# Kernel optimization log

Hardware: AMD Instinct MI355X
Metric: run time of the kernel (lower is better)

## Reference

```python
import jax, jax.numpy as jnp
import numpy as np

N = 40000   # nodes
E = 480000  # edges
F = 128     # input features
H = 128     # hidden
C = 10      # classes
G = 128     # graphs in batch
L = 3       # conv layers
EPS = 1e-5


def _bn(x, g, b):
    # BatchNorm1d, training-mode batch statistics (biased variance, as torch)
    m = x.mean(0)
    v = x.var(0)
    return (x - m) / jnp.sqrt(v + EPS) * g + b


def _gcn_prop(x, row, col, w, n):
    # PyG-style GCN propagation: add self loops (weight 1), sym-normalize, scatter-add.
    loop = jnp.arange(n)
    r = jnp.concatenate([row, loop])
    c = jnp.concatenate([col, loop])
    ww = jnp.concatenate([w, jnp.ones((n,), x.dtype)])
    deg = jax.ops.segment_sum(ww, r, num_segments=n)  # deg >= 1 thanks to self loops
    dinv = jnp.power(deg, -0.5)
    norm = dinv[r] * ww * dinv[c]                      # [E+N]
    return jax.ops.segment_sum(norm[:, None] * x[r], c, num_segments=n)


def setup_inputs() -> dict:
    key = jax.random.key(0)
    ks = jax.random.split(key, 12)
    nrm = lambda k, s: jax.random.normal(k, s, jnp.float32) * 0.02
    return {
        'x': jax.random.normal(ks[0], (N, F), jnp.float32),
        'edge_index': jax.random.randint(ks[1], (2, E), 0, N, jnp.int32),
        'batch': jnp.sort(jax.random.randint(ks[2], (N,), 0, G, jnp.int32)),
        'bn_feat_g': jnp.ones((F,), jnp.float32), 'bn_feat_b': jnp.full((F,), 1e-4, jnp.float32),
        'W_feat': nrm(ks[3], (F, H)),
        'bns_g': jnp.ones((L, H), jnp.float32), 'bns_b': jnp.full((L, H), 1e-4, jnp.float32),
        'conv_W': nrm(ks[4], (L, H, H)), 'conv_b': jnp.zeros((L, H), jnp.float32),
        'W_eatt': nrm(ks[5], (2 * H, 2)), 'b_eatt': jnp.zeros((2,), jnp.float32),
        'W_natt': nrm(ks[6], (H, 2)), 'b_natt': jnp.zeros((2,), jnp.float32),
        'bnc_g': jnp.ones((H,), jnp.float32), 'bnc_b': jnp.full((H,), 1e-4, jnp.float32),
        'bno_g': jnp.ones((H,), jnp.float32), 'bno_b': jnp.full((H,), 1e-4, jnp.float32),
        'Wc': nrm(ks[7], (H, H)), 'bc': jnp.zeros((H,), jnp.float32),
        'Wo': nrm(ks[8], (H, H)), 'bo': jnp.zeros((H,), jnp.float32),
        'ro_bn1_g': jnp.ones((3, H), jnp.float32), 'ro_bn1_b': jnp.full((3, H), 1e-4, jnp.float32),
        'ro_W1': nrm(ks[9], (3, H, H)), 'ro_b1': jnp.zeros((3, H), jnp.float32),
        'ro_bn2_g': jnp.ones((3, H), jnp.float32), 'ro_bn2_b': jnp.full((3, H), 1e-4, jnp.float32),
        'ro_W2': nrm(ks[10], (3, H, C)), 'ro_b2': jnp.zeros((3, C), jnp.float32),
    }


def reference(x, edge_index, batch,
              bn_feat_g, bn_feat_b, W_feat, bns_g, bns_b, conv_W, conv_b,
              W_eatt, b_eatt, W_natt, b_natt, bnc_g, bnc_b, bno_g, bno_b,
              Wc, bc, Wo, bo,
              ro_bn1_g, ro_bn1_b, ro_W1, ro_b1, ro_bn2_g, ro_bn2_b, ro_W2, ro_b2):
    row, col = edge_index[0], edge_index[1]
    # feature BN + gfn conv (linear only, no propagation, no bias) + ReLU
    h = jax.nn.relu(_bn(x, bn_feat_g, bn_feat_b) @ W_feat)
    ones_w = jnp.ones((E,), h.dtype)
    for i in range(L):
        z = _bn(h, bns_g[i], bns_b[i]) @ conv_W[i]
        h = jax.nn.relu(_gcn_prop(z, row, col, ones_w, N) + conv_b[i])
    # edge / node attention
    edge_rep = jnp.concatenate([h[row], h[col]], axis=-1)          # [E, 2H]
    e_att = jax.nn.softmax(edge_rep @ W_eatt + b_eatt, axis=-1)    # [E, 2]
    n_att = jax.nn.softmax(h @ W_natt + b_natt, axis=-1)           # [N, 2]
    xc = n_att[:, 0:1] * h
    xo = n_att[:, 1:2] * h
    xc = jax.nn.relu(_gcn_prop(_bn(xc, bnc_g, bnc_b) @ Wc, row, col, e_att[:, 0], N) + bc)
    xo = jax.nn.relu(_gcn_prop(_bn(xo, bno_g, bno_b) @ Wo, row, col, e_att[:, 1], N) + bo)
    # global add pool -> [G, H]
    xc = jax.ops.segment_sum(xc, batch, num_segments=G)
    xo = jax.ops.segment_sum(xo, batch, num_segments=G)

    def ro(v, i):
        v = _bn(v, ro_bn1_g[i], ro_bn1_b[i]) @ ro_W1[i] + ro_b1[i]
        v = _bn(jax.nn.relu(v), ro_bn2_g[i], ro_bn2_b[i]) @ ro_W2[i] + ro_b2[i]
        return jax.nn.log_softmax(v, axis=-1)

    # with_random=False -> identity permutation; cat_or_add='add' -> xc + xo
    return ro(xc, 0), ro(xo, 1), ro(xc + xo, 2)
```

## Files before the change

### kernel.cpp

```cpp
#include <hip/hip_runtime.h>

#define HD 128

typedef __attribute__((ext_vector_type(8))) short bf16x8v;
typedef __attribute__((ext_vector_type(4))) float f32x4v;

__device__ __forceinline__ unsigned short f2bf(float f) {
  unsigned int u = __float_as_uint(f);
  u += 0x7FFFu + ((u >> 16) & 1u);
  return (unsigned short)(u >> 16);
}
__device__ __forceinline__ float bf2f(unsigned short h) {
  return __uint_as_float(((unsigned int)h) << 16);
}
__device__ __forceinline__ float bflo(unsigned int u) { return __uint_as_float(u << 16); }
__device__ __forceinline__ float bfhi(unsigned int u) { return __uint_as_float(u & 0xFFFF0000u); }
__device__ __forceinline__ unsigned int packbf(float a, float b) {
  return (unsigned int)f2bf(a) | ((unsigned int)f2bf(b) << 16);
}


__global__ void hist_kernel(const int* __restrict__ row, const int* __restrict__ col,
                            int* __restrict__ cnt_in, int* __restrict__ outdeg, int e) {
  int i = blockIdx.x * blockDim.x + threadIdx.x;
  if (i < e) { atomicAdd(&cnt_in[col[i]], 1); atomicAdd(&outdeg[row[i]], 1); }
}

__global__ void scan1(const int* __restrict__ cnt, int n, int* __restrict__ sums) {
  __shared__ int lds[256];
  int b = blockIdx.x, t = threadIdx.x;
  int base = b * 1024 + t * 4;
  int s = 0;
#pragma unroll
  for (int m = 0; m < 4; m++) if (base + m < n) s += cnt[base + m];
  lds[t] = s;
  __syncthreads();
  for (int d = 128; d > 0; d >>= 1) {
    if (t < d) lds[t] += lds[t + d];
    __syncthreads();
  }
  if (t == 0) sums[b] = lds[0];
}

__global__ void scan2(const int* __restrict__ sums, int nc, int* __restrict__ off) {
  int l = threadIdx.x;
  int v = (l < nc) ? sums[l] : 0;
  int x = v;
#pragma unroll
  for (int d = 1; d < 64; d <<= 1) {
    int y = __shfl_up(x, d, 64);
    if (l >= d) x += y;
  }
  if (l < nc) off[l] = x - v;
}

__global__ void scan3(const int* __restrict__ cnt, int n, const int* __restrict__ off,
                      int* __restrict__ ptr, int* __restrict__ cursor) {
  __shared__ int lds[256];
  int b = blockIdx.x, t = threadIdx.x;
  int base = b * 1024 + t * 4;
  int v[4], p[4];
#pragma unroll
  for (int m = 0; m < 4; m++) v[m] = (base + m < n) ? cnt[base + m] : 0;
  p[0] = v[0];
#pragma unroll
  for (int m = 1; m < 4; m++) p[m] = p[m - 1] + v[m];
  int tsum = p[3];
  lds[t] = tsum;
  __syncthreads();
  for (int d = 1; d < 256; d <<= 1) {
    int y = 0;
    if (t >= d) y = lds[t - d];
    __syncthreads();
    lds[t] += y;
    __syncthreads();
  }
  int basev = off[b] + lds[t] - tsum;
  if (b == 0 && t == 0) ptr[0] = 0;
#pragma unroll
  for (int m = 0; m < 4; m++) {
    int i = base + m;
    if (i < n) {
      int incl = basev + p[m];
      ptr[i + 1] = incl;
      cursor[i] = incl - v[m];
    }
  }
}

__global__ void place1(const int* __restrict__ row, const int* __restrict__ col,
                       int* __restrict__ cursor, int* __restrict__ csr_src,
                       int* __restrict__ csr_dst, int* __restrict__ csr_eid, int e) {
  int i = blockIdx.x * blockDim.x + threadIdx.x;
  if (i < e) {
    int c = col[i];
    int pos = atomicAdd(&cursor[c], 1);
    csr_src[pos] = row[i];
    csr_dst[pos] = c;
    csr_eid[pos] = i;
  }
}

__global__ void place2(const int* __restrict__ row, int* __restrict__ cursor2,
                       int* __restrict__ csr2_eid, int e) {
  int i = blockIdx.x * blockDim.x + threadIdx.x;
  if (i < e) {
    int pos = atomicAdd(&cursor2[row[i]], 1);
    csr2_eid[pos] = i;
  }
}

__global__ void dinv1_kernel(const int* __restrict__ outdeg, float* __restrict__ dinv1, int n) {
  int i = blockIdx.x * blockDim.x + threadIdx.x;
  if (i < n) dinv1[i] = rsqrtf((float)(outdeg[i] + 1));
}

__global__ void wn1_flat(const int* __restrict__ csr_src, const int* __restrict__ csr_dst,
                         const float* __restrict__ dinv1, float* __restrict__ wn, int e) {
  int i = blockIdx.x * blockDim.x + threadIdx.x;
  if (i < e) wn[i] = dinv1[csr_src[i]] * dinv1[csr_dst[i]];
}


__global__ void colstats_castx(const float* __restrict__ A, unsigned short* __restrict__ Abf,
                               int n, int rpb, float* __restrict__ sum, float* __restrict__ sumsq) {
  int colj = threadIdx.x & (HD - 1);
  int half = threadIdx.x >> 7;
  int r0 = blockIdx.x * rpb;
  int r1 = min(n, r0 + rpb);
  float s = 0.f, q = 0.f;
  for (int r = r0 + half; r < r1; r += 2) {
    float v = A[(size_t)r * HD + colj];
    Abf[(size_t)r * HD + colj] = f2bf(v);
    s += v; q += v * v;
  }
  atomicAdd(&sum[colj], s);
  atomicAdd(&sumsq[colj], q);
}

__global__ void colstats_bf(const unsigned short* __restrict__ A, int n, int rpb,
                            float* __restrict__ sum, float* __restrict__ sumsq) {
  int colj = threadIdx.x & (HD - 1);
  int half = threadIdx.x >> 7;
  int r0 = blockIdx.x * rpb;
  int r1 = min(n, r0 + rpb);
  float s = 0.f, q = 0.f;
  for (int r = r0 + half; r < r1; r += 2) {
    float v = bf2f(A[(size_t)r * HD + colj]);
    s += v; q += v * v;
  }
  atomicAdd(&sum[colj], s);
  atomicAdd(&sumsq[colj], q);
}

__global__ void colstats_scaled(const unsigned short* __restrict__ A, const float* __restrict__ natt,
                                int n, int rpb, float* __restrict__ o4) {
  int colj = threadIdx.x & (HD - 1);
  int half = threadIdx.x >> 7;
  int r0 = blockIdx.x * rpb;
  int r1 = min(n, r0 + rpb);
  float sc = 0.f, qc = 0.f, so = 0.f, qo = 0.f;
  for (int r = r0 + half; r < r1; r += 2) {
    float v = bf2f(A[(size_t)r * HD + colj]);
    float a0 = natt[r * 2], a1 = natt[r * 2 + 1];
    float vc = a0 * v, vo = a1 * v;
    sc += vc; qc += vc * vc; so += vo; qo += vo * vo;
  }
  atomicAdd(&o4[colj], sc);
  atomicAdd(&o4[HD + colj], qc);
  atomicAdd(&o4[2 * HD + colj], so);
  atomicAdd(&o4[3 * HD + colj], qo);
}


__global__ __launch_bounds__(256) void gemm_mfma(
    const unsigned short* __restrict__ A, const float* __restrict__ W,
    const float* __restrict__ g, const float* __restrict__ b,
    const float* __restrict__ ssum, const float* __restrict__ ssq, float invN,
    const float* __restrict__ rowscale, int rsStride,
    unsigned short* __restrict__ out, int n, int relu) {
  __shared__ unsigned short WT[128][136];
  __shared__ float sA[HD], tA[HD], tb[HD];
  int tid = threadIdx.x;
  int r00 = blockIdx.x * 128;

  if (tid < HD) {
    float m = ssum[tid] * invN;
    float v = ssq[tid] * invN - m * m;
    float s = g[tid] * rsqrtf(v + 1e-5f);
    sA[tid] = s;
    tA[tid] = b[tid] - m * s;
  }
  __syncthreads();
  for (int idx = tid; idx < 4096; idx += 256) {
    int k = idx >> 5;
    int j4 = (idx & 31) * 4;
    float4 w = *(const float4*)(W + (size_t)k * 128 + j4);
    float s = sA[k];
    WT[j4 + 0][k] = f2bf(w.x * s);
    WT[j4 + 1][k] = f2bf(w.y * s);
    WT[j4 + 2][k] = f2bf(w.z * s);
    WT[j4 + 3][k] = f2bf(w.w * s);
  }
  if (tid < HD) {
    float acc = 0.f;
#pragma unroll 8
    for (int k = 0; k < HD; k++) acc += tA[k] * W[(size_t)k * 128 + tid];
    tb[tid] = acc;
  }
  __syncthreads();

  int w = tid >> 6;
  int l = tid & 63;
  int colb = l & 15;
  int kcb = l >> 4;

#pragma unroll
  for (int rt = 0; rt < 2; rt++) {
    int r0 = r00 + rt * 64;
    if (r0 >= n) break;
    int arow = r0 + w * 16 + colb;
    bool rowok = arow < n;

    f32x4v acc[8];
#pragma unroll
    for (int jt = 0; jt < 8; jt++) acc[jt] = (f32x4v){0.f, 0.f, 0.f, 0.f};

    const unsigned short* Ap = A + (size_t)(rowok ? arow : 0) * 128 + kcb * 8;
#pragma unroll
    for (int kit = 0; kit < 4; kit++) {
      bf16x8v a;
      if (rowok) a = *(const bf16x8v*)(Ap + kit * 32);
      else a = (bf16x8v){0, 0, 0, 0, 0, 0, 0, 0};
#pragma unroll
      for (int jt = 0; jt < 8; jt++) {
        bf16x8v bb = *(const bf16x8v*)&WT[jt * 16 + colb][kit * 32 + kcb * 8];
        acc[jt] = __builtin_amdgcn_mfma_f32_16x16x32_bf16(a, bb, acc[jt], 0, 0, 0);
      }
    }

    int rbase = r0 + w * 16 + kcb * 4;
    float rs[4];
#pragma unroll
    for (int i = 0; i < 4; i++)
      rs[i] = rowscale ? ((rbase + i < n) ? rowscale[(size_t)(rbase + i) * rsStride] : 0.f) : 1.f;
#pragma unroll
    for (int jt = 0; jt < 8; jt++) {
      int colj = jt * 16 + colb;
      float tbv = tb[colj];
#pragma unroll
      for (int i = 0; i < 4; i++) {
        int r = rbase + i;
        if (r < n) {
          float v = acc[jt][i] * rs[i] + tbv;
          if (relu) v = fmaxf(v, 0.f);
          out[(size_t)r * 128 + colj] = f2bf(v);
        }
      }
    }
  }
}


__global__ __launch_bounds__(256) void prop1(
    const unsigned short* __restrict__ z, const int* __restrict__ ptr,
    const int* __restrict__ src, const float* __restrict__ wn,
    const float* __restrict__ dinv, const float* __restrict__ bias,
    unsigned short* __restrict__ out, int n, int relu) {
  int node = blockIdx.x * 4 + (threadIdx.x >> 6);
  if (node >= n) return;
  int lane = threadIdx.x & 63;
  const unsigned int* zp = (const unsigned int*)z;
  float dn = dinv[node];
  float ws = dn * dn;
  unsigned int us = zp[(size_t)node * 64 + lane];
  float a0 = ws * bflo(us), a1 = ws * bfhi(us);
  int e = ptr[node], e1 = ptr[node + 1];
  for (; e + 3 < e1; e += 4) {
    int s0 = src[e], s1 = src[e + 1], s2 = src[e + 2], s3 = src[e + 3];
    float w0 = wn[e], w1 = wn[e + 1], w2 = wn[e + 2], w3 = wn[e + 3];
    unsigned int u0 = zp[(size_t)s0 * 64 + lane];
    unsigned int u1 = zp[(size_t)s1 * 64 + lane];
    unsigned int u2 = zp[(size_t)s2 * 64 + lane];
    unsigned int u3 = zp[(size_t)s3 * 64 + lane];
    a0 += w0 * bflo(u0) + w1 * bflo(u1) + w2 * bflo(u2) + w3 * bflo(u3);
    a1 += w0 * bfhi(u0) + w1 * bfhi(u1) + w2 * bfhi(u2) + w3 * bfhi(u3);
  }
  for (; e < e1; e++) {
    unsigned int u = zp[(size_t)src[e] * 64 + lane];
    float we = wn[e];
    a0 += we * bflo(u);
    a1 += we * bfhi(u);
  }
  a0 += bias[lane * 2];
  a1 += bias[lane * 2 + 1];
  if (relu) { a0 = fmaxf(a0, 0.f); a1 = fmaxf(a1, 0.f); }
  ((unsigned int*)out)[(size_t)node * 64 + lane] = packbf(a0, a1);
}

__global__ __launch_bounds__(256) void prop2(
    const unsigned short* __restrict__ z1, const unsigned short* __restrict__ z2,
    const int* __restrict__ ptr, const int* __restrict__ src,
    const float* __restrict__ wnc, const float* __restrict__ wno,
    const float2* __restrict__ ddeg, const float* __restrict__ bc,
    const float* __restrict__ bo, unsigned short* __restrict__ xc,
    unsigned short* __restrict__ xo, int n) {
  int node = blockIdx.x * 4 + (threadIdx.x >> 6);
  if (node >= n) return;
  int lane = threadIdx.x & 63;
  const unsigned int* z1p = (const unsigned int*)z1;
  const unsigned int* z2p = (const unsigned int*)z2;
  float2 dd = ddeg[node];
  float wsc = dd.x * dd.x, wso = dd.y * dd.y;
  unsigned int uc = z1p[(size_t)node * 64 + lane];
  unsigned int uo = z2p[(size_t)node * 64 + lane];
  float c0 = wsc * bflo(uc), c1 = wsc * bfhi(uc);
  float o0 = wso * bflo(uo), o1 = wso * bfhi(uo);
  int e = ptr[node], e1 = ptr[node + 1];
  for (; e + 1 < e1; e += 2) {
    int s0 = src[e], s1 = src[e + 1];
    float wc0 = wnc[e], wc1 = wnc[e + 1];
    float wo0 = wno[e], wo1 = wno[e + 1];
    unsigned int a0 = z1p[(size_t)s0 * 64 + lane];
    unsigned int b0 = z2p[(size_t)s0 * 64 + lane];
    unsigned int a1 = z1p[(size_t)s1 * 64 + lane];
    unsigned int b1 = z2p[(size_t)s1 * 64 + lane];
    c0 += wc0 * bflo(a0) + wc1 * bflo(a1);
    c1 += wc0 * bfhi(a0) + wc1 * bfhi(a1);
    o0 += wo0 * bflo(b0) + wo1 * bflo(b1);
    o1 += wo0 * bfhi(b0) + wo1 * bfhi(b1);
  }
  for (; e < e1; e++) {
    int s = src[e];
    float wc = wnc[e], wo = wno[e];
    unsigned int a = z1p[(size_t)s * 64 + lane];
    unsigned int b = z2p[(size_t)s * 64 + lane];
    c0 += wc * bflo(a); c1 += wc * bfhi(a);
    o0 += wo * bflo(b); o1 += wo * bfhi(b);
  }
  c0 = fmaxf(c0 + bc[lane * 2], 0.f);
  c1 = fmaxf(c1 + bc[lane * 2 + 1], 0.f);
  o0 = fmaxf(o0 + bo[lane * 2], 0.f);
  o1 = fmaxf(o1 + bo[lane * 2 + 1], 0.f);
  ((unsigned int*)xc)[(size_t)node * 64 + lane] = packbf(c0, c1);
  ((unsigned int*)xo)[(size_t)node * 64 + lane] = packbf(o0, o1);
}


__global__ void proj_kernel(const unsigned short* __restrict__ h, const float* __restrict__ We,
                            const float* __restrict__ Wn, const float* __restrict__ bn,
                            float* __restrict__ natt, float* __restrict__ pe, int n) {
  int gtid = blockIdx.x * blockDim.x + threadIdx.x;
  int wave = gtid >> 6;
  int lane = threadIdx.x & 63;
  int nwaves = (gridDim.x * blockDim.x) >> 6;
  for (int node = wave; node < n; node += nwaves) {
    float h0 = bf2f(h[(size_t)node * HD + lane]);
    float h1 = bf2f(h[(size_t)node * HD + 64 + lane]);
    float v[6];
    v[0] = h0 * We[lane * 2 + 0] + h1 * We[(64 + lane) * 2 + 0];
    v[1] = h0 * We[lane * 2 + 1] + h1 * We[(64 + lane) * 2 + 1];
    v[2] = h0 * We[(128 + lane) * 2 + 0] + h1 * We[(192 + lane) * 2 + 0];
    v[3] = h0 * We[(128 + lane) * 2 + 1] + h1 * We[(192 + lane) * 2 + 1];
    v[4] = h0 * Wn[lane * 2 + 0] + h1 * Wn[(64 + lane) * 2 + 0];
    v[5] = h0 * Wn[lane * 2 + 1] + h1 * Wn[(64 + lane) * 2 + 1];
#pragma unroll
    for (int m = 32; m > 0; m >>= 1) {
#pragma unroll
      for (int q = 0; q < 6; q++) v[q] += __shfl_xor(v[q], m, 64);
    }
    if (lane == 0) {
      float q0 = v[4] + bn[0], q1 = v[5] + bn[1];
      float mx = fmaxf(q0, q1);
      float e0 = expf(q0 - mx), e1 = expf(q1 - mx);
      float inv = 1.f / (e0 + e1);
      natt[node * 2 + 0] = e0 * inv;
      natt[node * 2 + 1] = e1 * inv;
      pe[node * 4 + 0] = v[0];
      pe[node * 4 + 1] = v[1];
      pe[node * 4 + 2] = v[2];
      pe[node * 4 + 3] = v[3];
    }
  }
}

__global__ void eatt_flat(const int* __restrict__ row, const int* __restrict__ col,
                          const float* __restrict__ pe, const float* __restrict__ be,
                          float2* __restrict__ eattO, int e) {
  int i = blockIdx.x * blockDim.x + threadIdx.x;
  if (i >= e) return;
  int r = row[i], c = col[i];
  float l0 = pe[r * 4 + 0] + pe[c * 4 + 2] + be[0];
  float l1 = pe[r * 4 + 1] + pe[c * 4 + 3] + be[1];
  float m = fmaxf(l0, l1);
  float e0 = expf(l0 - m), e1 = expf(l1 - m);
  float inv = 1.f / (e0 + e1);
  eattO[i] = make_float2(e0 * inv, e1 * inv);
}

__global__ void deg_kernel(const int* __restrict__ ptrR, const int* __restrict__ csr2_eid,
                           const float2* __restrict__ eattO, float2* __restrict__ ddeg, int n) {
  int gtid = blockIdx.x * blockDim.x + threadIdx.x;
  int node = gtid >> 6;
  int lane = threadIdx.x & 63;
  if (node >= n) return;
  int e0 = ptrR[node], e1 = ptrR[node + 1];
  float sc = 0.f, so = 0.f;
  for (int e = e0 + lane; e < e1; e += 64) {
    float2 at = eattO[csr2_eid[e]];
    sc += at.x; so += at.y;
  }
#pragma unroll
  for (int m = 32; m > 0; m >>= 1) {
    sc += __shfl_xor(sc, m, 64);
    so += __shfl_xor(so, m, 64);
  }
  if (lane == 0) ddeg[node] = make_float2(rsqrtf(1.f + sc), rsqrtf(1.f + so));
}

__global__ void wn_flat(const int* __restrict__ csr_src, const int* __restrict__ csr_dst,
                        const int* __restrict__ csr_eid, const float2* __restrict__ eattO,
                        const float2* __restrict__ ddeg, float* __restrict__ wnc,
                        float* __restrict__ wno, int e) {
  int i = blockIdx.x * blockDim.x + threadIdx.x;
  if (i >= e) return;
  int s = csr_src[i], c = csr_dst[i];
  float2 at = eattO[csr_eid[i]];
  float2 ds = ddeg[s], dc = ddeg[c];
  wnc[i] = ds.x * at.x * dc.x;
  wno[i] = ds.y * at.y * dc.y;
}


#define POOL_RPB 32

__global__ void pool_kernel(const unsigned short* __restrict__ xc,
                            const unsigned short* __restrict__ xo,
                            const int* __restrict__ batch, int n,
                            float* __restrict__ pc, float* __restrict__ po) {
  int j = threadIdx.x;
  int r0 = blockIdx.x * POOL_RPB;
  int r1 = min(n, r0 + POOL_RPB);
  if (r0 >= n) return;
  int g = batch[r0];
  float ac = 0.f, ao = 0.f;
  for (int r = r0; r < r1; r++) {
    int br = batch[r];
    if (br != g) {
      atomicAdd(&pc[g * HD + j], ac);
      atomicAdd(&po[g * HD + j], ao);
      ac = 0.f; ao = 0.f; g = br;
    }
    ac += bf2f(xc[(size_t)r * HD + j]);
    ao += bf2f(xo[(size_t)r * HD + j]);
  }
  atomicAdd(&pc[g * HD + j], ac);
  atomicAdd(&po[g * HD + j], ao);
}


__global__ __launch_bounds__(256) void head1(
    const float* __restrict__ pc, const float* __restrict__ po,
    const float* __restrict__ bn1g, const float* __restrict__ bn1b,
    const float* __restrict__ W1, const float* __restrict__ b1,
    float* __restrict__ Ybuf) {
  int t = blockIdx.x >> 2;
  int jt = blockIdx.x & 3;
  __shared__ float V[128][132];
  __shared__ float Wt[128][33];
  __shared__ float sA[128], tA[128];
  __shared__ float redS[2][128], redQ[2][128];
  int tid = threadIdx.x;

  for (int idx = tid; idx < 16384; idx += 256) {
    int r = idx >> 7, j = idx & 127;
    float v = (t == 0) ? pc[idx] : (t == 1) ? po[idx] : (pc[idx] + po[idx]);
    V[r][j] = v;
  }
  for (int idx = tid; idx < 4096; idx += 256) {
    int k = idx >> 5, c = idx & 31;
    Wt[k][c] = W1[(size_t)t * 16384 + k * 128 + jt * 32 + c];
  }
  __syncthreads();
  {
    int cj = tid & 127, ch = tid >> 7;
    float s = 0.f, q = 0.f;
    for (int r = ch * 64; r < ch * 64 + 64; r++) { float v = V[r][cj]; s += v; q += v * v; }
    redS[ch][cj] = s; redQ[ch][cj] = q;
  }
  __syncthreads();
  if (tid < 128) {
    float s = redS[0][tid] + redS[1][tid];
    float q = redQ[0][tid] + redQ[1][tid];
    float m = s * (1.f / 128.f), var = q * (1.f / 128.f) - m * m;
    float sc = bn1g[t * 128 + tid] * rsqrtf(var + 1e-5f);
    sA[tid] = sc; tA[tid] = bn1b[t * 128 + tid] - m * sc;
  }
  __syncthreads();
  for (int idx = tid; idx < 16384; idx += 256) {
    int r = idx >> 7, j = idx & 127;
    V[r][j] = V[r][j] * sA[j] + tA[j];
  }
  __syncthreads();
  int tr = tid >> 5, tc = tid & 31;
  float acc[16];
#pragma unroll
  for (int i = 0; i < 16; i++) acc[i] = 0.f;
  for (int k = 0; k < 128; k += 4) {
    float w0 = Wt[k][tc], w1 = Wt[k + 1][tc], w2 = Wt[k + 2][tc], w3 = Wt[k + 3][tc];
#pragma unroll
    for (int i = 0; i < 16; i++) {
      float4 v = *(float4*)&V[tr * 16 + i][k];
      acc[i] += v.x * w0 + v.y * w1 + v.z * w2 + v.w * w3;
    }
  }
  float bj = b1[t * 128 + jt * 32 + tc];
#pragma unroll
  for (int i = 0; i < 16; i++) {
    int r = tr * 16 + i;
    Ybuf[(size_t)t * 16384 + r * 128 + jt * 32 + tc] = fmaxf(acc[i] + bj, 0.f);
  }
}

__global__ __launch_bounds__(256) void head2(
    const float* __restrict__ Ybuf,
    const float* __restrict__ bn2g, const float* __restrict__ bn2b,
    const float* __restrict__ W2, const float* __restrict__ b2,
    float* __restrict__ out) {
  int t = blockIdx.x;
  __shared__ float Y[128][132];
  __shared__ float W2s[128][11];
  __shared__ float Z[128][12];
  __shared__ float sA[128], tA[128];
  __shared__ float redS[2][128], redQ[2][128];
  int tid = threadIdx.x;

  for (int idx = tid; idx < 16384; idx += 256) {
    int r = idx >> 7, j = idx & 127;
    Y[r][j] = Ybuf[(size_t)t * 16384 + idx];
  }
  for (int idx = tid; idx < 1280; idx += 256) {
    int k = idx / 10, c = idx % 10;
    W2s[k][c] = W2[(size_t)t * 1280 + idx];
  }
  __syncthreads();
  {
    int cj = tid & 127, ch = tid >> 7;
    float s = 0.f, q = 0.f;
    for (int r = ch * 64; r < ch * 64 + 64; r++) { float v = Y[r][cj]; s += v; q += v * v; }
    redS[ch][cj] = s; redQ[ch][cj] = q;
  }
  __syncthreads();
  if (tid < 128) {
    float s = redS[0][tid] + redS[1][tid];
    float q = redQ[0][tid] + redQ[1][tid];
    float m = s * (1.f / 128.f), var = q * (1.f / 128.f) - m * m;
    float sc = bn2g[t * 128 + tid] * rsqrtf(var + 1e-5f);
    sA[tid] = sc; tA[tid] = bn2b[t * 128 + tid] - m * sc;
  }
  __syncthreads();
  for (int idx = tid; idx < 16384; idx += 256) {
    int r = idx >> 7, j = idx & 127;
    Y[r][j] = Y[r][j] * sA[j] + tA[j];
  }
  __syncthreads();
  for (int idx = tid; idx < 1280; idx += 256) {
    int r = idx / 10, c = idx % 10;
    float acc = b2[t * 10 + c];
#pragma unroll 8
    for (int k = 0; k < 128; k++) acc += Y[r][k] * W2s[k][c];
    Z[r][c] = acc;
  }
  __syncthreads();
  if (tid < 128) {
    int r = tid;
    float m = -1e30f;
    for (int c = 0; c < 10; c++) m = fmaxf(m, Z[r][c]);
    float se = 0.f;
    for (int c = 0; c < 10; c++) se += expf(Z[r][c] - m);
    float lse = m + logf(se);
    for (int c = 0; c < 10; c++) out[t * 1280 + r * 10 + c] = Z[r][c] - lse;
  }
}


extern "C" void kernel_launch(void* const* d_in, const int* in_sizes, int n_in,
                              void* d_out, int out_size, void* d_ws, size_t ws_size,
                              hipStream_t stream) {
  const int N = in_sizes[0] / HD;
  const int E = in_sizes[1] / 2;
  const int G = out_size / 30;

  const float* x      = (const float*)d_in[0];
  const int*   ei     = (const int*)d_in[1];
  const int*   batch  = (const int*)d_in[2];
  const float* bnfg   = (const float*)d_in[3];
  const float* bnfb   = (const float*)d_in[4];
  const float* Wfeat  = (const float*)d_in[5];
  const float* bnsg   = (const float*)d_in[6];
  const float* bnsb   = (const float*)d_in[7];
  const float* convW  = (const float*)d_in[8];
  const float* convb  = (const float*)d_in[9];
  const float* Weatt  = (const float*)d_in[10];
  const float* beatt  = (const float*)d_in[11];
  const float* Wnatt  = (const float*)d_in[12];
  const float* bnatt  = (const float*)d_in[13];
  const float* bncg   = (const float*)d_in[14];
  const float* bncb   = (const float*)d_in[15];
  const float* bnog   = (const float*)d_in[16];
  const float* bnob   = (const float*)d_in[17];
  const float* Wc     = (const float*)d_in[18];
  const float* bc     = (const float*)d_in[19];
  const float* Wo     = (const float*)d_in[20];
  const float* bo     = (const float*)d_in[21];
  const float* robn1g = (const float*)d_in[22];
  const float* robn1b = (const float*)d_in[23];
  const float* roW1   = (const float*)d_in[24];
  const float* rob1   = (const float*)d_in[25];
  const float* robn2g = (const float*)d_in[26];
  const float* robn2b = (const float*)d_in[27];
  const float* roW2   = (const float*)d_in[28];
  const float* rob2   = (const float*)d_in[29];
  float* out = (float*)d_out;

  const int* row = ei;
  const int* col = ei + E;

  char* p = (char*)d_ws;
  auto alloc = [&](size_t bytes) -> void* {
    void* r = (void*)p;
    p += (bytes + 255) & ~(size_t)255;
    return r;
  };
  unsigned short* xbf = (unsigned short*)alloc((size_t)N * HD * 2);
  unsigned short* B0  = (unsigned short*)alloc((size_t)N * HD * 2);
  unsigned short* Xc  = (unsigned short*)alloc((size_t)N * HD * 2);
  unsigned short* Xo  = (unsigned short*)alloc((size_t)N * HD * 2);
  unsigned short* Z1  = (unsigned short*)alloc((size_t)N * HD * 2);
  unsigned short* Z2  = (unsigned short*)alloc((size_t)N * HD * 2);
  float2* eattO  = (float2*)alloc((size_t)E * 8);
  int*   csr_src = (int*)alloc((size_t)E * 4);
  int*   csr_dst = (int*)alloc((size_t)E * 4);
  int*   csr_eid = (int*)alloc((size_t)E * 4);
  int*   csr2_eid= (int*)alloc((size_t)E * 4);
  float* wn1     = (float*)alloc((size_t)E * 4);
  float* wnc     = (float*)alloc((size_t)E * 4);
  float* wno     = (float*)alloc((size_t)E * 4);
  int*   ptrA    = (int*)alloc((size_t)(N + 1) * 4);
  int*   ptrR    = (int*)alloc((size_t)(N + 1) * 4);
  int*   cursor  = (int*)alloc((size_t)N * 4);
  int*   cursor2 = (int*)alloc((size_t)N * 4);
  int*   cnt_in  = (int*)alloc((size_t)N * 4);
  int*   outdeg  = (int*)alloc((size_t)N * 4);
  float* dinv1   = (float*)alloc((size_t)N * 4);
  float2* ddeg   = (float2*)alloc((size_t)N * 8);
  float* natt    = (float*)alloc((size_t)N * 2 * 4);
  float* pe      = (float*)alloc((size_t)N * 4 * 4);
  float* stats   = (float*)alloc(12 * HD * 4);
  float* pooledc = (float*)alloc((size_t)G * HD * 4);
  float* pooledo = (float*)alloc((size_t)G * HD * 4);
  float* Ybuf    = (float*)alloc((size_t)3 * 128 * 128 * 4);
  int*   csums   = (int*)alloc(64 * 4);
  int*   coffs   = (int*)alloc(64 * 4);
  int*   csums2  = (int*)alloc(64 * 4);
  int*   coffs2  = (int*)alloc(64 * 4);

  const int NCH = (N + 1023) / 1024;

  hipMemsetAsync(cnt_in, 0, (size_t)N * 4, stream);
  hipMemsetAsync(outdeg, 0, (size_t)N * 4, stream);
  hipMemsetAsync(stats, 0, 12 * HD * 4, stream);
  hipMemsetAsync(pooledc, 0, (size_t)G * HD * 4, stream);
  hipMemsetAsync(pooledo, 0, (size_t)G * HD * 4, stream);

  hist_kernel<<<(E + 255) / 256, 256, 0, stream>>>(row, col, cnt_in, outdeg, E);
  scan1<<<NCH, 256, 0, stream>>>(cnt_in, N, csums);
  scan2<<<1, 64, 0, stream>>>(csums, NCH, coffs);
  scan3<<<NCH, 256, 0, stream>>>(cnt_in, N, coffs, ptrA, cursor);
  scan1<<<NCH, 256, 0, stream>>>(outdeg, N, csums2);
  scan2<<<1, 64, 0, stream>>>(csums2, NCH, coffs2);
  scan3<<<NCH, 256, 0, stream>>>(outdeg, N, coffs2, ptrR, cursor2);
  place1<<<(E + 255) / 256, 256, 0, stream>>>(row, col, cursor, csr_src, csr_dst, csr_eid, E);
  place2<<<(E + 255) / 256, 256, 0, stream>>>(row, cursor2, csr2_eid, E);
  dinv1_kernel<<<(N + 255) / 256, 256, 0, stream>>>(outdeg, dinv1, N);
  wn1_flat<<<(E + 255) / 256, 256, 0, stream>>>(csr_src, csr_dst, dinv1, wn1, E);

  const int SB = 256;
  int rpb = (N + SB - 1) / SB;
  int gblocks = (N + 127) / 128;
  int pblocks = (N + 3) / 4;
  float invN = 1.f / (float)N;

  colstats_castx<<<SB, 256, 0, stream>>>(x, xbf, N, rpb, stats, stats + HD);
  gemm_mfma<<<gblocks, 256, 0, stream>>>(xbf, Wfeat, bnfg, bnfb, stats, stats + HD, invN,
                                         nullptr, 0, B0, N, 1);

  for (int i = 0; i < 3; i++) {
    float* hs = stats + 2 * HD + i * 2 * HD;
    colstats_bf<<<SB, 256, 0, stream>>>(B0, N, rpb, hs, hs + HD);
    gemm_mfma<<<gblocks, 256, 0, stream>>>(B0, convW + (size_t)i * HD * HD,
                                           bnsg + i * HD, bnsb + i * HD, hs, hs + HD, invN,
                                           nullptr, 0, Z1, N, 0);
    prop1<<<pblocks, 256, 0, stream>>>(Z1, ptrA, csr_src, wn1, dinv1,
                                       convb + i * HD, B0, N, 1);
  }

  proj_kernel<<<512, 256, 0, stream>>>(B0, Weatt, Wnatt, bnatt, natt, pe, N);
  eatt_flat<<<(E + 255) / 256, 256, 0, stream>>>(row, col, pe, beatt, eattO, E);
  deg_kernel<<<(N * 64 + 255) / 256, 256, 0, stream>>>(ptrR, csr2_eid, eattO, ddeg, N);
  wn_flat<<<(E + 255) / 256, 256, 0, stream>>>(csr_src, csr_dst, csr_eid, eattO, ddeg,
                                               wnc, wno, E);

  float* cs = stats + 8 * HD;
  colstats_scaled<<<SB, 256, 0, stream>>>(B0, natt, N, rpb, cs);
  gemm_mfma<<<gblocks, 256, 0, stream>>>(B0, Wc, bncg, bncb, cs, cs + HD, invN,
                                         natt, 2, Z1, N, 0);
  gemm_mfma<<<gblocks, 256, 0, stream>>>(B0, Wo, bnog, bnob, cs + 2 * HD, cs + 3 * HD, invN,
                                         natt + 1, 2, Z2, N, 0);

  prop2<<<pblocks, 256, 0, stream>>>(Z1, Z2, ptrA, csr_src, wnc, wno, ddeg, bc, bo,
                                     Xc, Xo, N);

  pool_kernel<<<(N + POOL_RPB - 1) / POOL_RPB, 128, 0, stream>>>(Xc, Xo, batch, N, pooledc, pooledo);
  head1<<<12, 256, 0, stream>>>(pooledc, pooledo, robn1g, robn1b, roW1, rob1, Ybuf);
  head2<<<3, 256, 0, stream>>>(Ybuf, robn2g, robn2b, roW2, rob2, out);
}
```

Baseline: 784.9 us.

## Vectorize column-stats kernels, merge CSR placement kernels, register-cache projection weights

New measurement: 702.4 us. -10.5%, faster.

```diff
diff --git a/kernel.cpp b/kernel.cpp
--- a/kernel.cpp
+++ b/kernel.cpp
@@ -88,25 +88,19 @@
   }
 }
 
-__global__ void place1(const int* __restrict__ row, const int* __restrict__ col,
-                       int* __restrict__ cursor, int* __restrict__ csr_src,
-                       int* __restrict__ csr_dst, int* __restrict__ csr_eid, int e) {
+__global__ void place_both(const int* __restrict__ row, const int* __restrict__ col,
+                           int* __restrict__ cursor, int* __restrict__ cursor2,
+                           int* __restrict__ csr_src, int* __restrict__ csr_dst,
+                           int* __restrict__ csr_eid, int* __restrict__ csr2_eid, int e) {
   int i = blockIdx.x * blockDim.x + threadIdx.x;
   if (i < e) {
-    int c = col[i];
+    int r = row[i], c = col[i];
     int pos = atomicAdd(&cursor[c], 1);
-    csr_src[pos] = row[i];
+    csr_src[pos] = r;
     csr_dst[pos] = c;
     csr_eid[pos] = i;
-  }
-}
-
-__global__ void place2(const int* __restrict__ row, int* __restrict__ cursor2,
-                       int* __restrict__ csr2_eid, int e) {
-  int i = blockIdx.x * blockDim.x + threadIdx.x;
-  if (i < e) {
-    int pos = atomicAdd(&cursor2[row[i]], 1);
-    csr2_eid[pos] = i;
+    int pos2 = atomicAdd(&cursor2[r], 1);
+    csr2_eid[pos2] = i;
   }
 }
 
@@ -122,54 +116,101 @@
 }
 
 
-__global__ void colstats_castx(const float* __restrict__ A, unsigned short* __restrict__ Abf,
-                               int n, int rpb, float* __restrict__ sum, float* __restrict__ sumsq) {
-  int colj = threadIdx.x & (HD - 1);
-  int half = threadIdx.x >> 7;
-  int r0 = blockIdx.x * rpb;
-  int r1 = min(n, r0 + rpb);
-  float s = 0.f, q = 0.f;
-  for (int r = r0 + half; r < r1; r += 2) {
-    float v = A[(size_t)r * HD + colj];
-    Abf[(size_t)r * HD + colj] = f2bf(v);
-    s += v; q += v * v;
-  }
-  atomicAdd(&sum[colj], s);
-  atomicAdd(&sumsq[colj], q);
-}
-
-__global__ void colstats_bf(const unsigned short* __restrict__ A, int n, int rpb,
-                            float* __restrict__ sum, float* __restrict__ sumsq) {
-  int colj = threadIdx.x & (HD - 1);
-  int half = threadIdx.x >> 7;
-  int r0 = blockIdx.x * rpb;
-  int r1 = min(n, r0 + rpb);
-  float s = 0.f, q = 0.f;
-  for (int r = r0 + half; r < r1; r += 2) {
-    float v = bf2f(A[(size_t)r * HD + colj]);
-    s += v; q += v * v;
-  }
-  atomicAdd(&sum[colj], s);
-  atomicAdd(&sumsq[colj], q);
-}
-
-__global__ void colstats_scaled(const unsigned short* __restrict__ A, const float* __restrict__ natt,
-                                int n, int rpb, float* __restrict__ o4) {
-  int colj = threadIdx.x & (HD - 1);
-  int half = threadIdx.x >> 7;
-  int r0 = blockIdx.x * rpb;
-  int r1 = min(n, r0 + rpb);
-  float sc = 0.f, qc = 0.f, so = 0.f, qo = 0.f;
-  for (int r = r0 + half; r < r1; r += 2) {
-    float v = bf2f(A[(size_t)r * HD + colj]);
-    float a0 = natt[r * 2], a1 = natt[r * 2 + 1];
-    float vc = a0 * v, vo = a1 * v;
-    sc += vc; qc += vc * vc; so += vo; qo += vo * vo;
-  }
-  atomicAdd(&o4[colj], sc);
-  atomicAdd(&o4[HD + colj], qc);
-  atomicAdd(&o4[2 * HD + colj], so);
-  atomicAdd(&o4[3 * HD + colj], qo);
+#define CS_BLOCKS 512
+
+__global__ __launch_bounds__(256) void colstats_castx(
+    const float* __restrict__ A, unsigned short* __restrict__ Abf, int n,
+    float* __restrict__ sum, float* __restrict__ sumsq) {
+  __shared__ float redS[8][132], redQ[8][132];
+  int tid = threadIdx.x;
+  int cg = tid & 31, ro = tid >> 5;
+  float s[4] = {0.f, 0.f, 0.f, 0.f}, q[4] = {0.f, 0.f, 0.f, 0.f};
+  for (int r = blockIdx.x * 8 + ro; r < n; r += gridDim.x * 8) {
+    float4 v = *(const float4*)(A + (size_t)r * HD + cg * 4);
+    uint2 pk;
+    pk.x = packbf(v.x, v.y);
+    pk.y = packbf(v.z, v.w);
+    *(uint2*)(Abf + (size_t)r * HD + cg * 4) = pk;
+    s[0] += v.x; q[0] += v.x * v.x;
+    s[1] += v.y; q[1] += v.y * v.y;
+    s[2] += v.z; q[2] += v.z * v.z;
+    s[3] += v.w; q[3] += v.w * v.w;
+  }
+#pragma unroll
+  for (int i = 0; i < 4; i++) { redS[ro][cg * 4 + i] = s[i]; redQ[ro][cg * 4 + i] = q[i]; }
+  __syncthreads();
+  if (tid < 128) {
+    float ts = 0.f, tq = 0.f;
+#pragma unroll
+    for (int k = 0; k < 8; k++) { ts += redS[k][tid]; tq += redQ[k][tid]; }
+    atomicAdd(&sum[tid], ts);
+    atomicAdd(&sumsq[tid], tq);
+  }
+}
+
+__global__ __launch_bounds__(256) void colstats_bf(
+    const unsigned short* __restrict__ A, int n,
+    float* __restrict__ sum, float* __restrict__ sumsq) {
+  __shared__ float redS[8][132], redQ[8][132];
+  int tid = threadIdx.x;
+  int cg = tid & 31, ro = tid >> 5;
+  float s[4] = {0.f, 0.f, 0.f, 0.f}, q[4] = {0.f, 0.f, 0.f, 0.f};
+  for (int r = blockIdx.x * 8 + ro; r < n; r += gridDim.x * 8) {
+    uint2 u = *(const uint2*)(A + (size_t)r * HD + cg * 4);
+    float v0 = bflo(u.x), v1 = bfhi(u.x), v2 = bflo(u.y), v3 = bfhi(u.y);
+    s[0] += v0; q[0] += v0 * v0;
+    s[1] += v1; q[1] += v1 * v1;
+    s[2] += v2; q[2] += v2 * v2;
+    s[3] += v3; q[3] += v3 * v3;
+  }
+#pragma unroll
+  for (int i = 0; i < 4; i++) { redS[ro][cg * 4 + i] = s[i]; redQ[ro][cg * 4 + i] = q[i]; }
+  __syncthreads();
+  if (tid < 128) {
+    float ts = 0.f, tq = 0.f;
+#pragma unroll
+    for (int k = 0; k < 8; k++) { ts += redS[k][tid]; tq += redQ[k][tid]; }
+    atomicAdd(&sum[tid], ts);
+    atomicAdd(&sumsq[tid], tq);
+  }
+}
+
+__global__ __launch_bounds__(256) void colstats_scaled(
+    const unsigned short* __restrict__ A, const float* __restrict__ natt, int n,
+    float* __restrict__ o4) {
+  __shared__ float rSC[8][132], rQC[8][132], rSO[8][132], rQO[8][132];
+  int tid = threadIdx.x;
+  int cg = tid & 31, ro = tid >> 5;
+  float sc[4] = {0.f, 0.f, 0.f, 0.f}, qc[4] = {0.f, 0.f, 0.f, 0.f};
+  float so[4] = {0.f, 0.f, 0.f, 0.f}, qo[4] = {0.f, 0.f, 0.f, 0.f};
+  for (int r = blockIdx.x * 8 + ro; r < n; r += gridDim.x * 8) {
+    uint2 u = *(const uint2*)(A + (size_t)r * HD + cg * 4);
+    float2 at = *(const float2*)(natt + r * 2);
+    float v[4] = {bflo(u.x), bfhi(u.x), bflo(u.y), bfhi(u.y)};
+#pragma unroll
+    for (int i = 0; i < 4; i++) {
+      float vc = at.x * v[i], vo = at.y * v[i];
+      sc[i] += vc; qc[i] += vc * vc;
+      so[i] += vo; qo[i] += vo * vo;
+    }
+  }
+#pragma unroll
+  for (int i = 0; i < 4; i++) {
+    rSC[ro][cg * 4 + i] = sc[i]; rQC[ro][cg * 4 + i] = qc[i];
+    rSO[ro][cg * 4 + i] = so[i]; rQO[ro][cg * 4 + i] = qo[i];
+  }
+  __syncthreads();
+  if (tid < 128) {
+    float a = 0.f, b = 0.f, c = 0.f, d = 0.f;
+#pragma unroll
+    for (int k = 0; k < 8; k++) {
+      a += rSC[k][tid]; b += rQC[k][tid]; c += rSO[k][tid]; d += rQO[k][tid];
+    }
+    atomicAdd(&o4[tid], a);
+    atomicAdd(&o4[HD + tid], b);
+    atomicAdd(&o4[2 * HD + tid], c);
+    atomicAdd(&o4[3 * HD + tid], d);
+  }
 }
 
 
@@ -354,16 +395,20 @@
   int wave = gtid >> 6;
   int lane = threadIdx.x & 63;
   int nwaves = (gridDim.x * blockDim.x) >> 6;
+  const unsigned int* hp = (const unsigned int*)h;
+  float4 we0 = *(const float4*)(We + lane * 4);
+  float4 we1 = *(const float4*)(We + 256 + lane * 4);
+  float4 wn0 = *(const float4*)(Wn + lane * 4);
   for (int node = wave; node < n; node += nwaves) {
-    float h0 = bf2f(h[(size_t)node * HD + lane]);
-    float h1 = bf2f(h[(size_t)node * HD + 64 + lane]);
+    unsigned int u = hp[(size_t)node * 64 + lane];
+    float h0 = bflo(u), h1 = bfhi(u);
     float v[6];
-    v[0] = h0 * We[lane * 2 + 0] + h1 * We[(64 + lane) * 2 + 0];
-    v[1] = h0 * We[lane * 2 + 1] + h1 * We[(64 + lane) * 2 + 1];
-    v[2] = h0 * We[(128 + lane) * 2 + 0] + h1 * We[(192 + lane) * 2 + 0];
-    v[3] = h0 * We[(128 + lane) * 2 + 1] + h1 * We[(192 + lane) * 2 + 1];
-    v[4] = h0 * Wn[lane * 2 + 0] + h1 * Wn[(64 + lane) * 2 + 0];
-    v[5] = h0 * Wn[lane * 2 + 1] + h1 * Wn[(64 + lane) * 2 + 1];
+    v[0] = h0 * we0.x + h1 * we0.z;
+    v[1] = h0 * we0.y + h1 * we0.w;
+    v[2] = h0 * we1.x + h1 * we1.z;
+    v[3] = h0 * we1.y + h1 * we1.w;
+    v[4] = h0 * wn0.x + h1 * wn0.z;
+    v[5] = h0 * wn0.y + h1 * wn0.w;
 #pragma unroll
     for (int m = 32; m > 0; m >>= 1) {
 #pragma unroll
@@ -680,24 +725,22 @@
   scan1<<<NCH, 256, 0, stream>>>(outdeg, N, csums2);
   scan2<<<1, 64, 0, stream>>>(csums2, NCH, coffs2);
   scan3<<<NCH, 256, 0, stream>>>(outdeg, N, coffs2, ptrR, cursor2);
-  place1<<<(E + 255) / 256, 256, 0, stream>>>(row, col, cursor, csr_src, csr_dst, csr_eid, E);
-  place2<<<(E + 255) / 256, 256, 0, stream>>>(row, cursor2, csr2_eid, E);
+  place_both<<<(E + 255) / 256, 256, 0, stream>>>(row, col, cursor, cursor2,
+                                                  csr_src, csr_dst, csr_eid, csr2_eid, E);
   dinv1_kernel<<<(N + 255) / 256, 256, 0, stream>>>(outdeg, dinv1, N);
   wn1_flat<<<(E + 255) / 256, 256, 0, stream>>>(csr_src, csr_dst, dinv1, wn1, E);
 
-  const int SB = 256;
-  int rpb = (N + SB - 1) / SB;
   int gblocks = (N + 127) / 128;
   int pblocks = (N + 3) / 4;
   float invN = 1.f / (float)N;
 
-  colstats_castx<<<SB, 256, 0, stream>>>(x, xbf, N, rpb, stats, stats + HD);
+  colstats_castx<<<CS_BLOCKS, 256, 0, stream>>>(x, xbf, N, stats, stats + HD);
   gemm_mfma<<<gblocks, 256, 0, stream>>>(xbf, Wfeat, bnfg, bnfb, stats, stats + HD, invN,
                                          nullptr, 0, B0, N, 1);
 
   for (int i = 0; i < 3; i++) {
     float* hs = stats + 2 * HD + i * 2 * HD;
-    colstats_bf<<<SB, 256, 0, stream>>>(B0, N, rpb, hs, hs + HD);
+    colstats_bf<<<CS_BLOCKS, 256, 0, stream>>>(B0, N, hs, hs + HD);
     gemm_mfma<<<gblocks, 256, 0, stream>>>(B0, convW + (size_t)i * HD * HD,
                                            bnsg + i * HD, bnsb + i * HD, hs, hs + HD, invN,
                                            nullptr, 0, Z1, N, 0);
@@ -712,7 +755,7 @@
                                                wnc, wno, E);
 
   float* cs = stats + 8 * HD;
-  colstats_scaled<<<SB, 256, 0, stream>>>(B0, natt, N, rpb, cs);
+  colstats_scaled<<<CS_BLOCKS, 256, 0, stream>>>(B0, natt, N, cs);
   gemm_mfma<<<gblocks, 256, 0, stream>>>(B0, Wc, bncg, bncb, cs, cs + HD, invN,
                                          natt, 2, Z1, N, 0);
   gemm_mfma<<<gblocks, 256, 0, stream>>>(B0, Wo, bnog, bnob, cs + 2 * HD, cs + 3 * HD, invN,
```
